# Kernel optimization log

Measured on AMD Instinct MI355X. Metric: run time of the kernel, lower is better.

The kernel has to match this reference:

```python
import jax, jax.numpy as jnp
import numpy as np

BATCH = 1024
INPUT_DIM = 4096
HV_DIM = 8192          # == 2**NUM_QUBITS, so encode_classical fully overwrites the state
NUM_QUBITS = 13
QUANTUM_DEPTH = 3


def setup_inputs() -> dict:
    key = jax.random.key(0)
    k1, k2, k3 = jax.random.split(key, 3)
    x = jax.random.normal(k1, (BATCH, INPUT_DIM), dtype=jnp.float32)
    # torch nn.Linear weight layout: [out_features, in_features]
    W = jax.random.normal(k2, (HV_DIM, INPUT_DIM), dtype=jnp.float32)
    quantum_params = jax.random.normal(k3, (QUANTUM_DEPTH, NUM_QUBITS), dtype=jnp.float32)
    return {"x": x, "W": W, "quantum_params": quantum_params}


def reference(x, W, quantum_params):
    # projection: classical_hv = x @ W^T  -> [B, HV_DIM]
    classical = x @ W.T
    # encode_classical: normalize, cast to complex, renormalize (second norm is 1;
    # kept for fidelity with the original code path)
    amps = (classical / jnp.linalg.norm(classical, axis=-1, keepdims=True)).astype(jnp.complex64)
    amps = amps / jnp.linalg.norm(amps, axis=-1, keepdims=True)

    # sequential gate sequence: for depth in range(D): for qubit in range(Q):
    #   amps = amps*cos(a/2) + roll(amps, 1)*sin(a/2)*1j
    # each step uses the updated amplitudes -> lax.scan over the flattened angles
    angles = quantum_params.reshape(-1)  # [D*Q], depth-major matching the loop order

    def step(a, angle):
        c = jnp.cos(angle * 0.5)
        s = jnp.sin(angle * 0.5)
        return a * c + jnp.roll(a, 1, axis=-1) * (s * 1j), None

    amps, _ = jax.lax.scan(step, amps, angles)
    return amps  # [B, 2**NUM_QUBITS] complex64 quantum amplitudes
```

## Files before the change

kernel.cpp:

```cpp
#include <hip/hip_runtime.h>
#include <hip/hip_fp16.h>
#include <math.h>

typedef _Float16 half8 __attribute__((ext_vector_type(8)));
typedef __fp16 fp16x2 __attribute__((ext_vector_type(2)));
typedef float f32x4 __attribute__((ext_vector_type(4)));

#define BATCH 1024
#define IN_DIM 4096
#define HV 8192
#define NTAP 40

#define BM 128
#define BN 128
#define BK 32
#define BKP 36

#define GLD16(g, l) __builtin_amdgcn_global_load_lds(                          \
    (const __attribute__((address_space(1))) void*)(g),                        \
    (__attribute__((address_space(3))) void*)(l), 16, 0, 0)

static __device__ __forceinline__ half8 pk8(f32x4 a, f32x4 b) {
    union { fp16x2 p[4]; half8 h; } u;
    u.p[0] = __builtin_amdgcn_cvt_pkrtz(a.x, a.y);
    u.p[1] = __builtin_amdgcn_cvt_pkrtz(a.z, a.w);
    u.p[2] = __builtin_amdgcn_cvt_pkrtz(b.x, b.y);
    u.p[3] = __builtin_amdgcn_cvt_pkrtz(b.z, b.w);
    return u.h;
}

typedef _Float16 half4v __attribute__((ext_vector_type(4)));
__global__ __launch_bounds__(256) void cvt_f32_f16(const float4* __restrict__ src,
                                                   half4v* __restrict__ dst, int n4) {
    int i = blockIdx.x * 256 + threadIdx.x;
    if (i < n4) {
        float4 v = src[i];
        half4v h;
        h.x = (_Float16)v.x; h.y = (_Float16)v.y;
        h.z = (_Float16)v.z; h.w = (_Float16)v.w;
        dst[i] = h;
    }
}

__global__ __launch_bounds__(64) void compute_taps(const float* __restrict__ qp,
                                                   float* __restrict__ taps) {
    const int lane = threadIdx.x;
    float qv = (lane < 39) ? qp[lane] : 0.f;
    float pr = (lane == 0) ? 1.f : 0.f;
    float pim = 0.f;
    for (int t = 0; t < 39; t++) {
        float a = __shfl(qv, t, 64) * 0.5f;
        float c = cosf(a), s = sinf(a);
        float ur = __shfl_up(pr, 1, 64);
        float ui = __shfl_up(pim, 1, 64);
        if (lane == 0) { ur = 0.f; ui = 0.f; }
        float nr = c * pr - s * ui;
        float ni = c * pim + s * ur;
        pr = nr; pim = ni;
    }
    if (lane < NTAP) taps[lane] = pr;
}

__global__ __launch_bounds__(256, 2) void gemm_f16(
        const _Float16* __restrict__ A,
        const _Float16* __restrict__ B,
        float* __restrict__ out,
        long out_n) {
    __shared__ __align__(16) _Float16 lgA[2][BM * BK];
    __shared__ __align__(16) _Float16 lgB[2][BN * BK];

    const int tid  = threadIdx.x;
    const int lane = tid & 63;
    const int wave = tid >> 6;
    const int wm = wave & 1;
    const int wn = wave >> 1;
    const int q = lane >> 4, r = lane & 15;
    const int bm = blockIdx.y * BM;
    const int bn = blockIdx.x * BN;

    const int srow  = tid >> 2;
    const int sslot = (tid & 3) ^ ((srow >> 1) & 3);
    const _Float16* gA0 = A + (size_t)(bm + srow) * IN_DIM + sslot * 8;
    const _Float16* gA1 = gA0 + (size_t)64 * IN_DIM;
    const _Float16* gB0 = B + (size_t)(bn + srow) * IN_DIM + sslot * 8;
    const _Float16* gB1 = gB0 + (size_t)64 * IN_DIM;
    const int d0 = (wave * 16) * BK;
    const int d1 = (64 + wave * 16) * BK;

    f32x4 acc[4][4] = {};

#define STAGE(buf, k0)  do {                         \
        GLD16(gA0 + (k0), &lgA[buf][d0]);            \
        GLD16(gA1 + (k0), &lgA[buf][d1]);            \
        GLD16(gB0 + (k0), &lgB[buf][d0]);            \
        GLD16(gB1 + (k0), &lgB[buf][d1]);            \
    } while (0)

#define COMPUTE(buf)  do {                                                         \
        half8 af[4], bf[4];                                                        \
        _Pragma("unroll")                                                          \
        for (int i = 0; i < 4; i++) {                                              \
            const int R = wm * 64 + i * 16 + r;                                    \
            af[i] = *(const half8*)&lgA[buf][R * BK + ((q ^ ((R >> 1) & 3)) * 8)]; \
        }                                                                          \
        _Pragma("unroll")                                                          \
        for (int j = 0; j < 4; j++) {                                              \
            const int R = wn * 64 + j * 16 + r;                                    \
            bf[j] = *(const half8*)&lgB[buf][R * BK + ((q ^ ((R >> 1) & 3)) * 8)]; \
        }                                                                          \
        _Pragma("unroll")                                                          \
        for (int i = 0; i < 4; i++)                                                \
            _Pragma("unroll")                                                      \
            for (int j = 0; j < 4; j++)                                            \
                acc[i][j] = __builtin_amdgcn_mfma_f32_16x16x32_f16(af[i], bf[j], acc[i][j], 0, 0, 0); \
    } while (0)

    STAGE(0, 0);
    __syncthreads();
    for (int k0 = 0; k0 < IN_DIM; k0 += 2 * BK) {
        STAGE(1, k0 + BK);
        COMPUTE(0);
        __syncthreads();
        if (k0 + 2 * BK < IN_DIM) STAGE(0, k0 + 2 * BK);
        COMPUTE(1);
        __syncthreads();
    }
#undef STAGE
#undef COMPUTE

    #pragma unroll
    for (int i = 0; i < 4; i++) {
        const int row = bm + wm * 64 + i * 16 + q * 4;
        #pragma unroll
        for (int j = 0; j < 4; j++) {
            const int col = bn + wn * 64 + j * 16 + r;
            #pragma unroll
            for (int reg = 0; reg < 4; reg++) {
                long idx = (long)(row + reg) * HV + col;
                if (idx < out_n) out[idx] = acc[i][j][reg];
            }
        }
    }
}

__global__ __launch_bounds__(256) void gemm_f32in(
        const float* __restrict__ A, const float* __restrict__ B,
        float* __restrict__ out, long out_n) {
    __shared__ __align__(16) float lgA[BM * BKP];
    __shared__ __align__(16) float lgB[BN * BKP];

    const int tid  = threadIdx.x;
    const int lane = tid & 63;
    const int wave = tid >> 6;
    const int wm = wave & 1, wn = wave >> 1;
    const int q = lane >> 4, r = lane & 15;
    const int bm = blockIdx.y * BM;
    const int bn = blockIdx.x * BN;

    const int rg = lane >> 3;
    const int cg = (lane & 7) * 4;
    const float* gA = A + (size_t)(bm + wave * 32 + rg) * IN_DIM + cg;
    const float* gB = B + (size_t)(bn + wave * 32 + rg) * IN_DIM + cg;
    float* lA = &lgA[(wave * 32 + rg) * BKP + cg];
    float* lB = &lgB[(wave * 32 + rg) * BKP + cg];

    f32x4 acc[4][4] = {};

    for (int k0 = 0; k0 < IN_DIM; k0 += BK) {
        float4 va[4], vb[4];
        #pragma unroll
        for (int i = 0; i < 4; i++) {
            va[i] = *(const float4*)(gA + k0 + (size_t)(8 * i) * IN_DIM);
            vb[i] = *(const float4*)(gB + k0 + (size_t)(8 * i) * IN_DIM);
        }
        __syncthreads();
        #pragma unroll
        for (int i = 0; i < 4; i++) {
            *(float4*)(lA + 8 * i * BKP) = va[i];
            *(float4*)(lB + 8 * i * BKP) = vb[i];
        }
        __syncthreads();

        half8 af[4], bf[4];
        #pragma unroll
        for (int i = 0; i < 4; i++) {
            const float* p = &lgA[(wm * 64 + i * 16 + r) * BKP + q * 8];
            af[i] = pk8(*(const f32x4*)p, *(const f32x4*)(p + 4));
        }
        #pragma unroll
        for (int j = 0; j < 4; j++) {
            const float* p = &lgB[(wn * 64 + j * 16 + r) * BKP + q * 8];
            bf[j] = pk8(*(const f32x4*)p, *(const f32x4*)(p + 4));
        }

        #pragma unroll
        for (int i = 0; i < 4; i++)
            #pragma unroll
            for (int j = 0; j < 4; j++)
                acc[i][j] = __builtin_amdgcn_mfma_f32_16x16x32_f16(af[i], bf[j], acc[i][j], 0, 0, 0);
    }

    #pragma unroll
    for (int i = 0; i < 4; i++) {
        const int row = bm + wm * 64 + i * 16 + q * 4;
        #pragma unroll
        for (int j = 0; j < 4; j++) {
            const int col = bn + wn * 64 + j * 16 + r;
            #pragma unroll
            for (int reg = 0; reg < 4; reg++) {
                long idx = (long)(row + reg) * HV + col;
                if (idx < out_n) out[idx] = acc[i][j][reg];
            }
        }
    }
}

#define SW4(p4) ((p4) ^ (((p4) >> 3) & 7))
__global__ __launch_bounds__(256) void norm_conv(float* __restrict__ out,
                                                 const float* __restrict__ qp,
                                                 const float* __restrict__ taps,
                                                 long out_n) {
    __shared__ __align__(16) float ldsv[40 + HV + 24];
    __shared__ float scr[NTAP];
    __shared__ float red[4];

    const int b = blockIdx.x;
    if ((long)(b + 1) * HV > out_n) return;

    const int tid = threadIdx.x;
    const int lane = tid & 63;
    const int wave = tid >> 6;
    float* rowp = out + (size_t)b * HV;
    const float4* row4 = (const float4*)rowp;
    float4* l4 = (float4*)ldsv;

    float ss = 0.f;
    #pragma unroll
    for (int it = 0; it < 8; it++) {
        int j = it * 256 + tid;
        float4 v = row4[j];
        ss += v.x * v.x + v.y * v.y + v.z * v.z + v.w * v.w;
        l4[SW4(10 + j)] = v;
    }
    if (tid < NTAP) {
        ldsv[(SW4(tid >> 2) << 2) | (tid & 3)] = rowp[HV - NTAP + tid];
    }

    #pragma unroll
    for (int off = 32; off > 0; off >>= 1) ss += __shfl_down(ss, off, 64);
    if (lane == 0) red[wave] = ss;

    if (taps) {
        if (tid < NTAP) scr[tid] = taps[tid];
    } else if (wave == 0) {
        float qv = (lane < 39) ? qp[lane] : 0.f;
        float pr = (lane == 0) ? 1.f : 0.f;
        float pim = 0.f;
        for (int t = 0; t < 39; t++) {
            float a = __shfl(qv, t, 64) * 0.5f;
            float c = cosf(a), s = sinf(a);
            float ur = __shfl_up(pr, 1, 64);
            float ui = __shfl_up(pim, 1, 64);
            if (lane == 0) { ur = 0.f; ui = 0.f; }
            float nr = c * pr - s * ui;
            float ni = c * pim + s * ur;
            pr = nr; pim = ni;
        }
        if (lane < NTAP) scr[lane] = pr;
    }
    __syncthreads();

    const float inv = 1.0f / sqrtf(red[0] + red[1] + red[2] + red[3]);

    float w[72];
    #pragma unroll
    for (int t = 0; t < 18; t++) ((float4*)w)[t] = l4[SW4(8 * tid + t)];

    float4* out4 = (float4*)rowp;
    #pragma unroll
    for (int h = 0; h < 2; h++) {
        float av[16] = {};
        #pragma unroll
        for (int k = 0; k < NTAP; k++) {
            const float c = scr[k];
            #pragma unroll
            for (int o = 0; o < 16; o++) av[o] += c * w[40 + h * 16 + o - k];
        }
        #pragma unroll
        for (int t = 0; t < 4; t++) {
            out4[8 * tid + 4 * h + t] = make_float4(inv * av[4 * t], inv * av[4 * t + 1],
                                                    inv * av[4 * t + 2], inv * av[4 * t + 3]);
        }
    }
}

extern "C" void kernel_launch(void* const* d_in, const int* in_sizes, int n_in,
                              void* d_out, int out_size, void* d_ws, size_t ws_size,
                              hipStream_t stream) {
    const float* x  = (const float*)d_in[0];
    const float* W  = (const float*)d_in[1];
    const float* qp = (const float*)d_in[2];
    float* out = (float*)d_out;
    long out_n = (long)out_size;

    const size_t need = (size_t)BATCH * IN_DIM * 2 + (size_t)HV * IN_DIM * 2;
    dim3 grid(HV / BN, BATCH / BM);

    if (ws_size >= need) {
        _Float16* xh = (_Float16*)d_ws;
        _Float16* wh = xh + (size_t)BATCH * IN_DIM;
        float* taps = nullptr;
        if (ws_size >= need + 256) {
            taps = (float*)((char*)d_ws + need);
            compute_taps<<<1, 64, 0, stream>>>(qp, taps);
        }
        int n4x = BATCH * IN_DIM / 4;
        int n4w = HV * IN_DIM / 4;
        cvt_f32_f16<<<n4x / 256, 256, 0, stream>>>((const float4*)x, (half4v*)xh, n4x);
        cvt_f32_f16<<<n4w / 256, 256, 0, stream>>>((const float4*)W, (half4v*)wh, n4w);
        gemm_f16<<<grid, 256, 0, stream>>>(xh, wh, out, out_n);
        norm_conv<<<BATCH, 256, 0, stream>>>(out, qp, taps, out_n);
    } else {
        float* taps = nullptr;
        if (ws_size >= 256) {
            taps = (float*)d_ws;
            compute_taps<<<1, 64, 0, stream>>>(qp, taps);
        }
        gemm_f32in<<<grid, 256, 0, stream>>>(x, W, out, out_n);
        norm_conv<<<BATCH, 256, 0, stream>>>(out, qp, taps, out_n);
    }
}
```

Measured before the change: 321.2 us.

## Enlarge fp16 GEMM tile to 128x256x64 with triple-buffered LDS pipeline

The fp16 GEMM moves from a 128x128x32 tile with 256 threads and double buffering to a 128x256x64 tile with 512 threads (8 waves). It uses a three-stage ring of LDS buffers filled by direct global-to-LDS loads, with an explicit vmcnt wait and one barrier per k-step instead of two. It also uses an XOR swizzle suited to 64-wide rows and raises wave priority around the MFMA block. The aim is more operand reuse per loaded byte, fewer barriers and better hiding of load latency. The cost is about 147KB of LDS per block, which allows only one block per CU and half as many blocks in the grid.

```diff
diff --git a/kernel.cpp b/kernel.cpp
--- a/kernel.cpp
+++ b/kernel.cpp
@@ -15,6 +15,14 @@
 #define BN 128
 #define BK 32
 #define BKP 36
+
+#define BM2 128
+#define BN2 256
+#define BK2 64
+#define NT2 (IN_DIM / BK2)
+#define ASZ (BM2 * BK2)
+#define BSZ (BN2 * BK2)
+#define TSZ (ASZ + BSZ)
 
 #define GLD16(g, l) __builtin_amdgcn_global_load_lds(                          \
     (const __attribute__((address_space(1))) void*)(g),                        \
@@ -61,13 +69,12 @@
     if (lane < NTAP) taps[lane] = pr;
 }
 
-__global__ __launch_bounds__(256, 2) void gemm_f16(
+__global__ __launch_bounds__(512, 2) void gemm_f16(
         const _Float16* __restrict__ A,
         const _Float16* __restrict__ B,
         float* __restrict__ out,
         long out_n) {
-    __shared__ __align__(16) _Float16 lgA[2][BM * BK];
-    __shared__ __align__(16) _Float16 lgB[2][BN * BK];
+    __shared__ __align__(16) _Float16 lds[3 * TSZ];
 
     const int tid  = threadIdx.x;
     const int lane = tid & 63;
@@ -75,56 +82,89 @@
     const int wm = wave & 1;
     const int wn = wave >> 1;
     const int q = lane >> 4, r = lane & 15;
-    const int bm = blockIdx.y * BM;
-    const int bn = blockIdx.x * BN;
-
-    const int srow  = tid >> 2;
-    const int sslot = (tid & 3) ^ ((srow >> 1) & 3);
-    const _Float16* gA0 = A + (size_t)(bm + srow) * IN_DIM + sslot * 8;
-    const _Float16* gA1 = gA0 + (size_t)64 * IN_DIM;
-    const _Float16* gB0 = B + (size_t)(bn + srow) * IN_DIM + sslot * 8;
-    const _Float16* gB1 = gB0 + (size_t)64 * IN_DIM;
-    const int d0 = (wave * 16) * BK;
-    const int d1 = (64 + wave * 16) * BK;
+    const int bm = blockIdx.y * BM2;
+    const int bn = blockIdx.x * BN2;
+
+    const _Float16* srcA[2];
+    int dA[2];
+    #pragma unroll
+    for (int h = 0; h < 2; h++) {
+        const int p = h * 512 + tid;
+        const int R = p >> 3, c = (p & 7) ^ (R & 7);
+        srcA[h] = A + (size_t)(bm + R) * IN_DIM + c * 8;
+        dA[h] = (h * 512 + wave * 64) * 8;
+    }
+    const _Float16* srcB[4];
+    int dB[4];
+    #pragma unroll
+    for (int h = 0; h < 4; h++) {
+        const int p = h * 512 + tid;
+        const int R = p >> 3, c = (p & 7) ^ (R & 7);
+        srcB[h] = B + (size_t)(bn + R) * IN_DIM + c * 8;
+        dB[h] = ASZ + (h * 512 + wave * 64) * 8;
+    }
 
     f32x4 acc[4][4] = {};
 
-#define STAGE(buf, k0)  do {                         \
-        GLD16(gA0 + (k0), &lgA[buf][d0]);            \
-        GLD16(gA1 + (k0), &lgA[buf][d1]);            \
-        GLD16(gB0 + (k0), &lgB[buf][d0]);            \
-        GLD16(gB1 + (k0), &lgB[buf][d1]);            \
+#define STAGE(u, k0)  do {                                   \
+        _Float16* bp = &lds[(u) * TSZ];                      \
+        GLD16(srcA[0] + (k0), bp + dA[0]);                   \
+        GLD16(srcA[1] + (k0), bp + dA[1]);                   \
+        GLD16(srcB[0] + (k0), bp + dB[0]);                   \
+        GLD16(srcB[1] + (k0), bp + dB[1]);                   \
+        GLD16(srcB[2] + (k0), bp + dB[2]);                   \
+        GLD16(srcB[3] + (k0), bp + dB[3]);                   \
     } while (0)
 
-#define COMPUTE(buf)  do {                                                         \
-        half8 af[4], bf[4];                                                        \
-        _Pragma("unroll")                                                          \
-        for (int i = 0; i < 4; i++) {                                              \
-            const int R = wm * 64 + i * 16 + r;                                    \
-            af[i] = *(const half8*)&lgA[buf][R * BK + ((q ^ ((R >> 1) & 3)) * 8)]; \
-        }                                                                          \
-        _Pragma("unroll")                                                          \
-        for (int j = 0; j < 4; j++) {                                              \
-            const int R = wn * 64 + j * 16 + r;                                    \
-            bf[j] = *(const half8*)&lgB[buf][R * BK + ((q ^ ((R >> 1) & 3)) * 8)]; \
-        }                                                                          \
-        _Pragma("unroll")                                                          \
-        for (int i = 0; i < 4; i++)                                                \
-            _Pragma("unroll")                                                      \
-            for (int j = 0; j < 4; j++)                                            \
-                acc[i][j] = __builtin_amdgcn_mfma_f32_16x16x32_f16(af[i], bf[j], acc[i][j], 0, 0, 0); \
+#define COMPUTE(u)  do {                                                            \
+        const _Float16* bp = &lds[(u) * TSZ];                                       \
+        half8 af[4][2], bf[4][2];                                                   \
+        _Pragma("unroll")                                                           \
+        for (int i = 0; i < 4; i++)                                                 \
+            _Pragma("unroll")                                                       \
+            for (int kk = 0; kk < 2; kk++) {                                        \
+                const int R = wm * 64 + i * 16 + r;                                 \
+                const int sw = (kk * 4 + q) ^ (r & 7);                              \
+                af[i][kk] = *(const half8*)&bp[R * 64 + sw * 8];                    \
+            }                                                                       \
+        _Pragma("unroll")                                                           \
+        for (int j = 0; j < 4; j++)                                                 \
+            _Pragma("unroll")                                                       \
+            for (int kk = 0; kk < 2; kk++) {                                        \
+                const int R = wn * 64 + j * 16 + r;                                 \
+                const int sw = (kk * 4 + q) ^ (r & 7);                              \
+                bf[j][kk] = *(const half8*)&bp[ASZ + R * 64 + sw * 8];              \
+            }                                                                       \
+        __builtin_amdgcn_s_setprio(1);                                              \
+        _Pragma("unroll")                                                           \
+        for (int i = 0; i < 4; i++)                                                 \
+            _Pragma("unroll")                                                       \
+            for (int j = 0; j < 4; j++)                                             \
+                _Pragma("unroll")                                                   \
+                for (int kk = 0; kk < 2; kk++)                                      \
+                    acc[i][j] = __builtin_amdgcn_mfma_f32_16x16x32_f16(             \
+                        af[i][kk], bf[j][kk], acc[i][j], 0, 0, 0);                  \
+        __builtin_amdgcn_s_setprio(0);                                              \
     } while (0)
 
     STAGE(0, 0);
-    __syncthreads();
-    for (int k0 = 0; k0 < IN_DIM; k0 += 2 * BK) {
-        STAGE(1, k0 + BK);
-        COMPUTE(0);
-        __syncthreads();
-        if (k0 + 2 * BK < IN_DIM) STAGE(0, k0 + 2 * BK);
-        COMPUTE(1);
-        __syncthreads();
-    }
+    STAGE(1, BK2);
+    int cur = 0;
+    for (int t = 0; t < NT2 - 1; ++t) {
+        asm volatile("s_waitcnt vmcnt(6)" ::: "memory");
+        __builtin_amdgcn_sched_barrier(0);
+        __builtin_amdgcn_s_barrier();
+        if (t + 2 < NT2) {
+            const int nxt = (cur + 2 >= 3) ? cur - 1 : cur + 2;
+            STAGE(nxt, (t + 2) * BK2);
+        }
+        COMPUTE(cur);
+        cur = (cur + 1 == 3) ? 0 : cur + 1;
+    }
+    asm volatile("s_waitcnt vmcnt(0)" ::: "memory");
+    __builtin_amdgcn_sched_barrier(0);
+    __builtin_amdgcn_s_barrier();
+    COMPUTE(cur);
 #undef STAGE
 #undef COMPUTE
 
@@ -304,7 +344,6 @@
     long out_n = (long)out_size;
 
     const size_t need = (size_t)BATCH * IN_DIM * 2 + (size_t)HV * IN_DIM * 2;
-    dim3 grid(HV / BN, BATCH / BM);
 
     if (ws_size >= need) {
         _Float16* xh = (_Float16*)d_ws;
@@ -318,7 +357,8 @@
         int n4w = HV * IN_DIM / 4;
         cvt_f32_f16<<<n4x / 256, 256, 0, stream>>>((const float4*)x, (half4v*)xh, n4x);
         cvt_f32_f16<<<n4w / 256, 256, 0, stream>>>((const float4*)W, (half4v*)wh, n4w);
-        gemm_f16<<<grid, 256, 0, stream>>>(xh, wh, out, out_n);
+        dim3 grid2(HV / BN2, BATCH / BM2);
+        gemm_f16<<<grid2, 512, 0, stream>>>(xh, wh, out, out_n);
         norm_conv<<<BATCH, 256, 0, stream>>>(out, qp, taps, out_n);
     } else {
         float* taps = nullptr;
@@ -326,6 +366,7 @@
             taps = (float*)d_ws;
             compute_taps<<<1, 64, 0, stream>>>(qp, taps);
         }
+        dim3 grid(HV / BN, BATCH / BM);
         gemm_f32in<<<grid, 256, 0, stream>>>(x, W, out, out_n);
         norm_conv<<<BATCH, 256, 0, stream>>>(out, qp, taps, out_n);
     }
```

New measurement: 303.5 us. 1.06x faster.
